# Kernel optimization log

Measured on AMD Instinct MI355X. Metric: run time of the kernel, lower is better.

Reference implementation:

```python
import jax, jax.numpy as jnp
import numpy as np


def setup_inputs() -> dict:
    key = jax.random.key(0)
    kx, kw = jax.random.split(key)
    x = jax.random.normal(kx, (32, 4096, 1024), dtype=jnp.float32)
    # torch init is rand*0.01 (all-positive, degenerate for sign); use randn*0.01
    # to emulate a trained BNN weight with mixed signs.
    weight = jax.random.normal(kw, (1024, 1024), dtype=jnp.float32) * 0.01
    return {"x": x, "weight": weight}


def reference(x, weight):
    # SignFunction forward: binarize weight to {-1, 0(+at exact 0), +1};
    # torch.sign semantics -> jnp.sign. F.linear(x, W) = x @ W.T
    b_weight = jnp.sign(weight)  # [out, in]
    return jnp.einsum('bsi,oi->bso', x, b_weight)
```

## Files before the change

kernel.cpp:

```cpp
#include <hip/hip_runtime.h>
#include <hip/hip_bf16.h>


typedef __attribute__((ext_vector_type(8))) short bf16x8;
typedef __attribute__((ext_vector_type(4))) float f32x4;

#define BM 128
#define BN 128
#define BK 64
#define KDIM 1024
#define NDIM 1024
#define NKSTEP (KDIM / BK)

__device__ __forceinline__ unsigned cvt2(float a, float b) {
  unsigned r;
  asm("v_cvt_pk_bf16_f32 %0, %1, %2" : "=v"(r) : "v"(a), "v"(b));
  return r;
}

__global__ void sign_kernel(const float4* __restrict__ W, ushort4* __restrict__ Bs, int n4) {
  int i = blockIdx.x * blockDim.x + threadIdx.x;
  if (i >= n4) return;
  float4 v = W[i];
  const float* pv = (const float*)&v;
  ushort4 r;
  unsigned short* pr = (unsigned short*)&r;
#pragma unroll
  for (int j = 0; j < 4; ++j) {
    union { float f; unsigned int u; } c; c.f = pv[j];
    pr[j] = ((c.u & 0x7fffffffu) == 0u)
                ? (unsigned short)0
                : (unsigned short)(0x3f80u | ((c.u >> 16) & 0x8000u));
  }
  Bs[i] = r;
}

__global__ __launch_bounds__(256, 3) void bgemm_kernel(
    const float* __restrict__ X,
    const unsigned short* __restrict__ Bs,
    float* __restrict__ O) {
  __shared__ f32x4 sA[BM * 16];
  __shared__ unsigned short sB[BN * BK];

  const int t = threadIdx.x;
  const int l = t & 63;
  const int w = t >> 6;
  const int wr = w >> 1;
  const int wc = w & 1;

  const unsigned nwg = gridDim.x;
  unsigned swz = blockIdx.x;
  if ((nwg & 7u) == 0u) swz = (blockIdx.x & 7u) * (nwg >> 3) + (blockIdx.x >> 3);
  const int bm = (int)(swz >> 3);
  const int bn = (int)(swz & 7u);
  const size_t m0 = (size_t)bm * BM;
  const int N0 = bn * BN;

  const float* agp[8];
#pragma unroll
  for (int i = 0; i < 8; ++i) {
    int c = i * 256 + t;
    int r = c >> 4;
    int q = (c & 15) ^ (r & 15);
    agp[i] = X + (m0 + (size_t)r) * KDIM + q * 4;
  }

  const unsigned short* bgp[4];
#pragma unroll
  for (int i = 0; i < 4; ++i) {
    int c = i * 256 + t;
    int n = c >> 3;
    int q = (c & 7) ^ (n & 7);
    bgp[i] = Bs + (size_t)(N0 + n) * KDIM + q * 8;
  }

  const int ll = l & 15;
  const int kb = l >> 4;
  int idxA[2][4];
  int offB[2][4];
#pragma unroll
  for (int ks = 0; ks < 2; ++ks) {
#pragma unroll
    for (int i = 0; i < 4; ++i) {
      int row = wr * 64 + i * 16 + ll;
      idxA[ks][i] = row * 16 + ((ks * 8 + kb * 2) ^ (row & 15));
    }
#pragma unroll
    for (int j = 0; j < 4; ++j) {
      int n = wc * 64 + j * 16 + ll;
      offB[ks][j] = n * 64 + (((ks * 4 + kb) ^ (n & 7)) * 8);
    }
  }

  f32x4 acc[4][4];
#pragma unroll
  for (int i = 0; i < 4; ++i)
#pragma unroll
    for (int j = 0; j < 4; ++j) acc[i][j] = (f32x4)0.0f;

  for (int kk = 0; kk < NKSTEP; ++kk) {
    const int k0 = kk * BK;
#pragma unroll
    for (int i = 0; i < 8; ++i)
      __builtin_amdgcn_global_load_lds(
          (const __attribute__((address_space(1))) void*)(agp[i] + k0),
          (__attribute__((address_space(3))) void*)(&sA[i * 256 + t]), 16, 0, 0);
#pragma unroll
    for (int i = 0; i < 4; ++i)
      __builtin_amdgcn_global_load_lds(
          (const __attribute__((address_space(1))) void*)(bgp[i] + k0),
          (__attribute__((address_space(3))) void*)(&sB[(i * 256 + t) * 8]), 16, 0, 0);
    asm volatile("s_waitcnt vmcnt(0) lgkmcnt(0)" ::: "memory");
    __syncthreads();

#pragma unroll
    for (int ks = 0; ks < 2; ++ks) {
      bf16x8 bv[4];
#pragma unroll
      for (int j = 0; j < 4; ++j)
        bv[j] = *reinterpret_cast<const bf16x8*>(sB + offB[ks][j]);
      bf16x8 av[4];
#pragma unroll
      for (int i = 0; i < 4; ++i) {
        f32x4 c0 = sA[idxA[ks][i]];
        f32x4 c1 = sA[idxA[ks][i] ^ 1];
        union { uint4 u; bf16x8 v; } cv;
        cv.u.x = cvt2(c0.x, c0.y); cv.u.y = cvt2(c0.z, c0.w);
        cv.u.z = cvt2(c1.x, c1.y); cv.u.w = cvt2(c1.z, c1.w);
        av[i] = cv.v;
      }
#pragma unroll
      for (int i = 0; i < 4; ++i)
#pragma unroll
        for (int j = 0; j < 4; ++j)
          acc[i][j] = __builtin_amdgcn_mfma_f32_16x16x32_bf16(
              av[i], bv[j], acc[i][j], 0, 0, 0);
    }
    __syncthreads();
  }

  const int crow = kb * 4;
#pragma unroll
  for (int i = 0; i < 4; ++i) {
    const size_t r0 = m0 + wr * 64 + i * 16 + crow;
#pragma unroll
    for (int j = 0; j < 4; ++j) {
      const int col = N0 + wc * 64 + j * 16 + ll;
      float* op = O + r0 * NDIM + col;
#pragma unroll
      for (int e = 0; e < 4; ++e) op[(size_t)e * NDIM] = acc[i][j][e];
    }
  }
}

__global__ void naive_kernel(const float* __restrict__ X, const float* __restrict__ W,
                             float* __restrict__ O, long long total) {
  long long idx = (long long)blockIdx.x * blockDim.x + threadIdx.x;
  if (idx >= total) return;
  int n = (int)(idx & (NDIM - 1));
  long long m = idx >> 10;
  const float* xr = X + m * KDIM;
  const float* wr = W + (long long)n * KDIM;
  float s = 0.f;
  for (int k = 0; k < KDIM; ++k) {
    float wv = wr[k];
    float sg = (wv > 0.f) ? 1.f : ((wv < 0.f) ? -1.f : 0.f);
    s += xr[k] * sg;
  }
  O[idx] = s;
}

extern "C" void kernel_launch(void* const* d_in, const int* in_sizes, int n_in,
                              void* d_out, int out_size, void* d_ws, size_t ws_size,
                              hipStream_t stream) {
  const float* X = (const float*)d_in[0];
  const float* W = (const float*)d_in[1];
  float* O = (float*)d_out;
  const long long M = (long long)in_sizes[0] / KDIM;

  const size_t need_ws = (size_t)NDIM * KDIM * sizeof(unsigned short);
  if (ws_size >= need_ws && (M % BM) == 0) {
    unsigned short* Bs = (unsigned short*)d_ws;
    int n4 = (NDIM * KDIM) / 4;
    sign_kernel<<<dim3(n4 / 256), dim3(256), 0, stream>>>(
        (const float4*)W, (ushort4*)Bs, n4);
    dim3 grid((unsigned)((M / BM) * (NDIM / BN)));
    bgemm_kernel<<<grid, dim3(256), 0, stream>>>(X, Bs, O);
  } else {
    long long total = M * NDIM;
    long long blocks = (total + 255) / 256;
    naive_kernel<<<dim3((unsigned)blocks), dim3(256), 0, stream>>>(X, W, O, total);
  }
}
```

Baseline: 429.1 us.

## Double-buffer LDS tiles with BK=32 to overlap global loads and MFMA

```diff
diff --git a/kernel.cpp b/kernel.cpp
--- a/kernel.cpp
+++ b/kernel.cpp
@@ -7,7 +7,7 @@
 
 #define BM 128
 #define BN 128
-#define BK 64
+#define BK 32
 #define KDIM 1024
 #define NDIM 1024
 #define NKSTEP (KDIM / BK)
@@ -39,8 +39,8 @@
     const float* __restrict__ X,
     const unsigned short* __restrict__ Bs,
     float* __restrict__ O) {
-  __shared__ f32x4 sA[BM * 16];
-  __shared__ unsigned short sB[BN * BK];
+  __shared__ f32x4 sA[2][BM * 8];
+  __shared__ unsigned short sB[2][BN * BK];
 
   const int t = threadIdx.x;
   const int l = t & 63;
@@ -56,40 +56,38 @@
   const size_t m0 = (size_t)bm * BM;
   const int N0 = bn * BN;
 
-  const float* agp[8];
-#pragma unroll
-  for (int i = 0; i < 8; ++i) {
-    int c = i * 256 + t;
-    int r = c >> 4;
-    int q = (c & 15) ^ (r & 15);
-    agp[i] = X + (m0 + (size_t)r) * KDIM + q * 4;
-  }
-
-  const unsigned short* bgp[4];
+  const float* agp[4];
 #pragma unroll
   for (int i = 0; i < 4; ++i) {
     int c = i * 256 + t;
-    int n = c >> 3;
-    int q = (c & 7) ^ (n & 7);
+    int r = c >> 3;
+    int q = (c & 7) ^ (r & 7);
+    agp[i] = X + (m0 + (size_t)r) * KDIM + q * 4;
+  }
+
+  const unsigned short* bgp[2];
+#pragma unroll
+  for (int i = 0; i < 2; ++i) {
+    int c = i * 256 + t;
+    int n = c >> 2;
+    int q = (c & 3) ^ ((n >> 1) & 3);
     bgp[i] = Bs + (size_t)(N0 + n) * KDIM + q * 8;
   }
 
   const int ll = l & 15;
   const int kb = l >> 4;
-  int idxA[2][4];
-  int offB[2][4];
-#pragma unroll
-  for (int ks = 0; ks < 2; ++ks) {
-#pragma unroll
-    for (int i = 0; i < 4; ++i) {
-      int row = wr * 64 + i * 16 + ll;
-      idxA[ks][i] = row * 16 + ((ks * 8 + kb * 2) ^ (row & 15));
-    }
-#pragma unroll
-    for (int j = 0; j < 4; ++j) {
-      int n = wc * 64 + j * 16 + ll;
-      offB[ks][j] = n * 64 + (((ks * 4 + kb) ^ (n & 7)) * 8);
-    }
+  int idxA[4];
+#pragma unroll
+  for (int i = 0; i < 4; ++i) {
+    int row = wr * 64 + i * 16 + ll;
+    idxA[i] = row * 8 + ((kb * 2) ^ (row & 7));
+  }
+  int offB[4];
+#pragma unroll
+  for (int j = 0; j < 4; ++j) {
+    int n = wc * 64 + j * 16 + ll;
+    int q = kb ^ ((n >> 1) & 3);
+    offB[j] = n * BK + q * 8;
   }
 
   f32x4 acc[4][4];
@@ -98,46 +96,56 @@
 #pragma unroll
     for (int j = 0; j < 4; ++j) acc[i][j] = (f32x4)0.0f;
 
-  for (int kk = 0; kk < NKSTEP; ++kk) {
-    const int k0 = kk * BK;
-#pragma unroll
-    for (int i = 0; i < 8; ++i)
-      __builtin_amdgcn_global_load_lds(
-          (const __attribute__((address_space(1))) void*)(agp[i] + k0),
-          (__attribute__((address_space(3))) void*)(&sA[i * 256 + t]), 16, 0, 0);
-#pragma unroll
-    for (int i = 0; i < 4; ++i)
-      __builtin_amdgcn_global_load_lds(
-          (const __attribute__((address_space(1))) void*)(bgp[i] + k0),
-          (__attribute__((address_space(3))) void*)(&sB[(i * 256 + t) * 8]), 16, 0, 0);
-    asm volatile("s_waitcnt vmcnt(0) lgkmcnt(0)" ::: "memory");
-    __syncthreads();
-
-#pragma unroll
-    for (int ks = 0; ks < 2; ++ks) {
-      bf16x8 bv[4];
-#pragma unroll
-      for (int j = 0; j < 4; ++j)
-        bv[j] = *reinterpret_cast<const bf16x8*>(sB + offB[ks][j]);
-      bf16x8 av[4];
-#pragma unroll
-      for (int i = 0; i < 4; ++i) {
-        f32x4 c0 = sA[idxA[ks][i]];
-        f32x4 c1 = sA[idxA[ks][i] ^ 1];
-        union { uint4 u; bf16x8 v; } cv;
-        cv.u.x = cvt2(c0.x, c0.y); cv.u.y = cvt2(c0.z, c0.w);
-        cv.u.z = cvt2(c1.x, c1.y); cv.u.w = cvt2(c1.z, c1.w);
-        av[i] = cv.v;
-      }
-#pragma unroll
-      for (int i = 0; i < 4; ++i)
-#pragma unroll
-        for (int j = 0; j < 4; ++j)
-          acc[i][j] = __builtin_amdgcn_mfma_f32_16x16x32_bf16(
-              av[i], bv[j], acc[i][j], 0, 0, 0);
-    }
-    __syncthreads();
-  }
+#define STAGE(buf, k0)                                                         \
+  do {                                                                         \
+    _Pragma("unroll") for (int i = 0; i < 4; ++i)                              \
+        __builtin_amdgcn_global_load_lds(                                      \
+            (const __attribute__((address_space(1))) void*)(agp[i] + (k0)),    \
+            (__attribute__((address_space(3))) void*)(&sA[buf][i * 256 + t]),  \
+            16, 0, 0);                                                         \
+    _Pragma("unroll") for (int i = 0; i < 2; ++i)                              \
+        __builtin_amdgcn_global_load_lds(                                      \
+            (const __attribute__((address_space(1))) void*)(bgp[i] + (k0)),    \
+            (__attribute__((address_space(3))) void*)(&sB[buf][(i * 256 + t) * 8]), \
+            16, 0, 0);                                                         \
+  } while (0)
+
+  STAGE(0, 0);
+  asm volatile("s_waitcnt vmcnt(0) lgkmcnt(0)" ::: "memory");
+  __syncthreads();
+
+#define STEP(CUR)                                                              \
+  {                                                                            \
+    if (kk + 1 < NKSTEP) STAGE((CUR) ^ 1, (kk + 1) * BK);                      \
+    const unsigned short* sb = sB[CUR];                                        \
+    bf16x8 bv[4];                                                              \
+    _Pragma("unroll") for (int j = 0; j < 4; ++j)                              \
+        bv[j] = *reinterpret_cast<const bf16x8*>(sb + offB[j]);                \
+    bf16x8 av[4];                                                              \
+    _Pragma("unroll") for (int i = 0; i < 4; ++i) {                            \
+      f32x4 c0 = sA[CUR][idxA[i]];                                             \
+      f32x4 c1 = sA[CUR][idxA[i] ^ 1];                                         \
+      union { uint4 u; bf16x8 v; } cv;                                         \
+      cv.u.x = cvt2(c0.x, c0.y); cv.u.y = cvt2(c0.z, c0.w);                    \
+      cv.u.z = cvt2(c1.x, c1.y); cv.u.w = cvt2(c1.z, c1.w);                    \
+      av[i] = cv.v;                                                            \
+    }                                                                          \
+    _Pragma("unroll") for (int i = 0; i < 4; ++i)                              \
+        _Pragma("unroll") for (int j = 0; j < 4; ++j)                          \
+            acc[i][j] = __builtin_amdgcn_mfma_f32_16x16x32_bf16(               \
+                av[i], bv[j], acc[i][j], 0, 0, 0);                             \
+    asm volatile("s_waitcnt vmcnt(0)" ::: "memory");                           \
+    __syncthreads();                                                           \
+    ++kk;                                                                      \
+  }
+
+  int kk = 0;
+  while (kk < NKSTEP) {
+    STEP(0)
+    STEP(1)
+  }
+#undef STEP
+#undef STAGE
 
   const int crow = kb * 4;
 #pragma unroll
```

After: 540.7 us. 1.26x slower.

## Convert A tile to bf16 at load time and store padded bf16 in LDS

Applied to the files above, without the earlier changes.

```diff
diff --git a/kernel.cpp b/kernel.cpp
--- a/kernel.cpp
+++ b/kernel.cpp
@@ -11,6 +11,7 @@
 #define KDIM 1024
 #define NDIM 1024
 #define NKSTEP (KDIM / BK)
+#define LDA 72
 
 __device__ __forceinline__ unsigned cvt2(float a, float b) {
   unsigned r;
@@ -35,11 +36,11 @@
   Bs[i] = r;
 }
 
-__global__ __launch_bounds__(256, 3) void bgemm_kernel(
+__global__ __launch_bounds__(256, 4) void bgemm_kernel(
     const float* __restrict__ X,
     const unsigned short* __restrict__ Bs,
     float* __restrict__ O) {
-  __shared__ f32x4 sA[BM * 16];
+  __shared__ unsigned short sA[BM * LDA];
   __shared__ unsigned short sB[BN * BK];
 
   const int t = threadIdx.x;
@@ -56,34 +57,32 @@
   const size_t m0 = (size_t)bm * BM;
   const int N0 = bn * BN;
 
-  const float* agp[8];
-#pragma unroll
-  for (int i = 0; i < 8; ++i) {
-    int c = i * 256 + t;
-    int r = c >> 4;
-    int q = (c & 15) ^ (r & 15);
-    agp[i] = X + (m0 + (size_t)r) * KDIM + q * 4;
-  }
+  const int ar = t >> 1;
+  const int ah = t & 1;
+  const float* agl = X + (m0 + (size_t)ar) * KDIM + ah * 32;
+  const int awo = ar * LDA + ah * 32;
 
   const unsigned short* bgp[4];
+  int bw[4];
 #pragma unroll
   for (int i = 0; i < 4; ++i) {
     int c = i * 256 + t;
     int n = c >> 3;
     int q = (c & 7) ^ (n & 7);
     bgp[i] = Bs + (size_t)(N0 + n) * KDIM + q * 8;
+    bw[i] = c * 8;
   }
 
   const int ll = l & 15;
   const int kb = l >> 4;
-  int idxA[2][4];
+  int offA[2][4];
   int offB[2][4];
 #pragma unroll
   for (int ks = 0; ks < 2; ++ks) {
 #pragma unroll
     for (int i = 0; i < 4; ++i) {
       int row = wr * 64 + i * 16 + ll;
-      idxA[ks][i] = row * 16 + ((ks * 8 + kb * 2) ^ (row & 15));
+      offA[ks][i] = row * LDA + ks * 32 + kb * 8;
     }
 #pragma unroll
     for (int j = 0; j < 4; ++j) {
@@ -100,35 +99,41 @@
 
   for (int kk = 0; kk < NKSTEP; ++kk) {
     const int k0 = kk * BK;
-#pragma unroll
-    for (int i = 0; i < 8; ++i)
-      __builtin_amdgcn_global_load_lds(
-          (const __attribute__((address_space(1))) void*)(agp[i] + k0),
-          (__attribute__((address_space(3))) void*)(&sA[i * 256 + t]), 16, 0, 0);
+
+    const float4* ap = reinterpret_cast<const float4*>(agl + k0);
+    float4 f0 = ap[0], f1 = ap[1], f2 = ap[2], f3 = ap[3];
+    float4 f4 = ap[4], f5 = ap[5], f6 = ap[6], f7 = ap[7];
 #pragma unroll
     for (int i = 0; i < 4; ++i)
       __builtin_amdgcn_global_load_lds(
           (const __attribute__((address_space(1))) void*)(bgp[i] + k0),
-          (__attribute__((address_space(3))) void*)(&sB[(i * 256 + t) * 8]), 16, 0, 0);
+          (__attribute__((address_space(3))) void*)(&sB[bw[i]]), 16, 0, 0);
+    uint4 q0, q1, q2, q3;
+    q0.x = cvt2(f0.x, f0.y); q0.y = cvt2(f0.z, f0.w);
+    q0.z = cvt2(f1.x, f1.y); q0.w = cvt2(f1.z, f1.w);
+    q1.x = cvt2(f2.x, f2.y); q1.y = cvt2(f2.z, f2.w);
+    q1.z = cvt2(f3.x, f3.y); q1.w = cvt2(f3.z, f3.w);
+    q2.x = cvt2(f4.x, f4.y); q2.y = cvt2(f4.z, f4.w);
+    q2.z = cvt2(f5.x, f5.y); q2.w = cvt2(f5.z, f5.w);
+    q3.x = cvt2(f6.x, f6.y); q3.y = cvt2(f6.z, f6.w);
+    q3.z = cvt2(f7.x, f7.y); q3.w = cvt2(f7.z, f7.w);
+    *reinterpret_cast<uint4*>(&sA[awo]) = q0;
+    *reinterpret_cast<uint4*>(&sA[awo + 8]) = q1;
+    *reinterpret_cast<uint4*>(&sA[awo + 16]) = q2;
+    *reinterpret_cast<uint4*>(&sA[awo + 24]) = q3;
     asm volatile("s_waitcnt vmcnt(0) lgkmcnt(0)" ::: "memory");
     __syncthreads();
 
 #pragma unroll
     for (int ks = 0; ks < 2; ++ks) {
+      bf16x8 av[4];
       bf16x8 bv[4];
+#pragma unroll
+      for (int i = 0; i < 4; ++i)
+        av[i] = *reinterpret_cast<const bf16x8*>(sA + offA[ks][i]);
 #pragma unroll
       for (int j = 0; j < 4; ++j)
         bv[j] = *reinterpret_cast<const bf16x8*>(sB + offB[ks][j]);
-      bf16x8 av[4];
-#pragma unroll
-      for (int i = 0; i < 4; ++i) {
-        f32x4 c0 = sA[idxA[ks][i]];
-        f32x4 c1 = sA[idxA[ks][i] ^ 1];
-        union { uint4 u; bf16x8 v; } cv;
-        cv.u.x = cvt2(c0.x, c0.y); cv.u.y = cvt2(c0.z, c0.w);
-        cv.u.z = cvt2(c1.x, c1.y); cv.u.w = cvt2(c1.z, c1.w);
-        av[i] = cv.v;
-      }
 #pragma unroll
       for (int i = 0; i < 4; ++i)
 #pragma unroll
```

After: 693.4 us. +61.6%, slower.

## Load A fragments directly from global into registers, drop A LDS staging

Applied to the files above, without the earlier changes.

```diff
diff --git a/kernel.cpp b/kernel.cpp
--- a/kernel.cpp
+++ b/kernel.cpp
@@ -35,18 +35,15 @@
   Bs[i] = r;
 }
 
-__global__ __launch_bounds__(256, 3) void bgemm_kernel(
+__global__ __launch_bounds__(256) void bgemm_kernel(
     const float* __restrict__ X,
     const unsigned short* __restrict__ Bs,
     float* __restrict__ O) {
-  __shared__ f32x4 sA[BM * 16];
   __shared__ unsigned short sB[BN * BK];
 
   const int t = threadIdx.x;
   const int l = t & 63;
   const int w = t >> 6;
-  const int wr = w >> 1;
-  const int wc = w & 1;
 
   const unsigned nwg = gridDim.x;
   unsigned swz = blockIdx.x;
@@ -56,83 +53,80 @@
   const size_t m0 = (size_t)bm * BM;
   const int N0 = bn * BN;
 
-  const float* agp[8];
+  const int ll = l & 15;
+  const int kb = l >> 4;
+
+  const float* aglp[2];
 #pragma unroll
-  for (int i = 0; i < 8; ++i) {
-    int c = i * 256 + t;
-    int r = c >> 4;
-    int q = (c & 15) ^ (r & 15);
-    agp[i] = X + (m0 + (size_t)r) * KDIM + q * 4;
-  }
+  for (int i = 0; i < 2; ++i)
+    aglp[i] = X + (m0 + (size_t)(w * 32 + i * 16 + ll)) * KDIM + kb * 8;
 
   const unsigned short* bgp[4];
+  int bw[4];
 #pragma unroll
   for (int i = 0; i < 4; ++i) {
     int c = i * 256 + t;
     int n = c >> 3;
     int q = (c & 7) ^ (n & 7);
     bgp[i] = Bs + (size_t)(N0 + n) * KDIM + q * 8;
+    bw[i] = c * 8;
   }
 
-  const int ll = l & 15;
-  const int kb = l >> 4;
-  int idxA[2][4];
-  int offB[2][4];
+  int offB[2][8];
 #pragma unroll
-  for (int ks = 0; ks < 2; ++ks) {
+  for (int ks = 0; ks < 2; ++ks)
 #pragma unroll
-    for (int i = 0; i < 4; ++i) {
-      int row = wr * 64 + i * 16 + ll;
-      idxA[ks][i] = row * 16 + ((ks * 8 + kb * 2) ^ (row & 15));
+    for (int j = 0; j < 8; ++j) {
+      int n = j * 16 + ll;
+      offB[ks][j] = n * BK + (((ks * 4 + kb) ^ (n & 7)) * 8);
     }
+
+  f32x4 acc[2][8];
 #pragma unroll
-    for (int j = 0; j < 4; ++j) {
-      int n = wc * 64 + j * 16 + ll;
-      offB[ks][j] = n * 64 + (((ks * 4 + kb) ^ (n & 7)) * 8);
-    }
-  }
-
-  f32x4 acc[4][4];
+  for (int i = 0; i < 2; ++i)
 #pragma unroll
-  for (int i = 0; i < 4; ++i)
-#pragma unroll
-    for (int j = 0; j < 4; ++j) acc[i][j] = (f32x4)0.0f;
+    for (int j = 0; j < 8; ++j) acc[i][j] = (f32x4)0.0f;
 
   for (int kk = 0; kk < NKSTEP; ++kk) {
     const int k0 = kk * BK;
-#pragma unroll
-    for (int i = 0; i < 8; ++i)
-      __builtin_amdgcn_global_load_lds(
-          (const __attribute__((address_space(1))) void*)(agp[i] + k0),
-          (__attribute__((address_space(3))) void*)(&sA[i * 256 + t]), 16, 0, 0);
+
 #pragma unroll
     for (int i = 0; i < 4; ++i)
       __builtin_amdgcn_global_load_lds(
           (const __attribute__((address_space(1))) void*)(bgp[i] + k0),
-          (__attribute__((address_space(3))) void*)(&sB[(i * 256 + t) * 8]), 16, 0, 0);
+          (__attribute__((address_space(3))) void*)(&sB[bw[i]]), 16, 0, 0);
+    f32x4 alo[2][2], ahi[2][2];
+#pragma unroll
+    for (int ks = 0; ks < 2; ++ks)
+#pragma unroll
+      for (int i = 0; i < 2; ++i) {
+        const float* p = aglp[i] + k0 + ks * 32;
+        alo[ks][i] = *reinterpret_cast<const f32x4*>(p);
+        ahi[ks][i] = *reinterpret_cast<const f32x4*>(p + 4);
+      }
     asm volatile("s_waitcnt vmcnt(0) lgkmcnt(0)" ::: "memory");
     __syncthreads();
 
 #pragma unroll
     for (int ks = 0; ks < 2; ++ks) {
-      bf16x8 bv[4];
+      bf16x8 av[2];
 #pragma unroll
-      for (int j = 0; j < 4; ++j)
-        bv[j] = *reinterpret_cast<const bf16x8*>(sB + offB[ks][j]);
-      bf16x8 av[4];
-#pragma unroll
-      for (int i = 0; i < 4; ++i) {
-        f32x4 c0 = sA[idxA[ks][i]];
-        f32x4 c1 = sA[idxA[ks][i] ^ 1];
+      for (int i = 0; i < 2; ++i) {
         union { uint4 u; bf16x8 v; } cv;
-        cv.u.x = cvt2(c0.x, c0.y); cv.u.y = cvt2(c0.z, c0.w);
-        cv.u.z = cvt2(c1.x, c1.y); cv.u.w = cvt2(c1.z, c1.w);
+        cv.u.x = cvt2(alo[ks][i].x, alo[ks][i].y);
+        cv.u.y = cvt2(alo[ks][i].z, alo[ks][i].w);
+        cv.u.z = cvt2(ahi[ks][i].x, ahi[ks][i].y);
+        cv.u.w = cvt2(ahi[ks][i].z, ahi[ks][i].w);
         av[i] = cv.v;
       }
+      bf16x8 bv[8];
 #pragma unroll
-      for (int i = 0; i < 4; ++i)
+      for (int j = 0; j < 8; ++j)
+        bv[j] = *reinterpret_cast<const bf16x8*>(sB + offB[ks][j]);
 #pragma unroll
-        for (int j = 0; j < 4; ++j)
+      for (int i = 0; i < 2; ++i)
+#pragma unroll
+        for (int j = 0; j < 8; ++j)
           acc[i][j] = __builtin_amdgcn_mfma_f32_16x16x32_bf16(
               av[i], bv[j], acc[i][j], 0, 0, 0);
     }
@@ -141,11 +135,11 @@
 
   const int crow = kb * 4;
 #pragma unroll
-  for (int i = 0; i < 4; ++i) {
-    const size_t r0 = m0 + wr * 64 + i * 16 + crow;
+  for (int i = 0; i < 2; ++i) {
+    const size_t r0 = m0 + w * 32 + i * 16 + crow;
 #pragma unroll
-    for (int j = 0; j < 4; ++j) {
-      const int col = N0 + wc * 64 + j * 16 + ll;
+    for (int j = 0; j < 8; ++j) {
+      const int col = N0 + j * 16 + ll;
       float* op = O + r0 * NDIM + col;
 #pragma unroll
       for (int e = 0; e < 4; ++e) op[(size_t)e * NDIM] = acc[i][j][e];
```

New measurement: 662.9 us. +54.5%, slower.
